# Kernel optimization log

Measured on AMD Instinct MI355X. Metric: run time of the kernel, lower is better.

The kernel has to match this reference:

```python
import jax, jax.numpy as jnp
import numpy as np

B, S, H, G, W = 4, 4096, 1024, 256, 8
CHUNK = 1024
NUM_HEADS = 4


def _ln(x, g, b, eps=1e-5):
    m = jnp.mean(x, axis=-1, keepdims=True)
    v = jnp.var(x, axis=-1, keepdims=True)
    return (x - m) / jnp.sqrt(v + eps) * g + b


def setup_inputs() -> dict:
    key = jax.random.key(0)
    ks = jax.random.split(key, 16)
    Hm = H // 2
    return {
        "x": jax.random.normal(ks[0], (B, S, H), dtype=jnp.float32),
        # wavelet params
        "mother_wavelets": jax.random.normal(ks[1], (1, W, H, 1), dtype=jnp.float32) * 0.02,
        "scales": jnp.ones((1, W, 1, 1), dtype=jnp.float32),
        # coeff_mixer: Linear(W,H/2) -> LN -> GELU -> Linear(H/2,H)  (weights stored as (in,out))
        "mix_w1": jax.random.normal(ks[2], (W, Hm), dtype=jnp.float32) * 0.02,
        "mix_b1": jnp.zeros((Hm,), dtype=jnp.float32),
        "mix_ln_g": jnp.ones((Hm,), dtype=jnp.float32),
        "mix_ln_b": jnp.zeros((Hm,), dtype=jnp.float32),
        "mix_w2": jax.random.normal(ks[3], (Hm, H), dtype=jnp.float32) * 0.02,
        "mix_b2": jnp.zeros((H,), dtype=jnp.float32),
        # attention (no bias)
        "wq": jax.random.normal(ks[4], (H, H), dtype=jnp.float32) * 0.02,
        "wk": jax.random.normal(ks[5], (H, H), dtype=jnp.float32) * 0.02,
        "wv": jax.random.normal(ks[6], (H, H), dtype=jnp.float32) * 0.02,
        "wo": jax.random.normal(ks[7], (H, H), dtype=jnp.float32) * 0.02,
        # output_proj: LN -> Linear(H, G)
        "out_ln_g": jnp.ones((H,), dtype=jnp.float32),
        "out_ln_b": jnp.zeros((H,), dtype=jnp.float32),
        "out_w": jax.random.normal(ks[8], (H, G), dtype=jnp.float32) * 0.02,
        "out_b": jnp.zeros((G,), dtype=jnp.float32),
    }


def reference(x, mother_wavelets, scales, mix_w1, mix_b1, mix_ln_g, mix_ln_b,
              mix_w2, mix_b2, wq, wk, wv, wo, out_ln_g, out_ln_b, out_w, out_b):
    b, s, h = x.shape
    nc = s // CHUNK  # chunks are independent -> fold into batch
    xc = x.reshape(b * nc, CHUNK, h)

    # wavelet coeffs: conv1d with kernel length == channels reduces to a dot product
    norm = jnp.sqrt(jnp.sum(mother_wavelets ** 2, axis=2, keepdims=True))
    kern = (mother_wavelets / jnp.maximum(norm, 1e-12)) * jax.nn.sigmoid(scales)
    kern = kern[0, :, :, 0]  # (W, H)
    coeffs = jnp.einsum('bsh,wh->bsw', xc, kern)  # (b*nc, L, W)

    # coeff mixer
    hid = _ln(coeffs @ mix_w1 + mix_b1, mix_ln_g, mix_ln_b)
    mixed = jax.nn.gelu(hid, approximate=False) @ mix_w2 + mix_b2  # (b*nc, L, H)

    # multi-head attention within each chunk (eval mode -> no causal mask)
    hd = h // NUM_HEADS
    def heads(t):
        return t.reshape(-1, CHUNK, NUM_HEADS, hd).transpose(0, 2, 1, 3)
    q, k, v = heads(mixed @ wq), heads(mixed @ wk), heads(mixed @ wv)
    scores = jnp.einsum('bhqd,bhkd->bhqk', q, k) * (hd ** -0.5)
    attn = jax.nn.softmax(scores, axis=-1)
    o = jnp.einsum('bhqk,bhkd->bhqd', attn, v)
    o = o.transpose(0, 2, 1, 3).reshape(-1, CHUNK, h) @ wo

    # output projection with residual
    y = _ln(o + mixed, out_ln_g, out_ln_b) @ out_w + out_b  # (b*nc, L, G)
    return y.reshape(b, s, -1)
```

## Files before the change

### kernel.cpp

```cpp
#include <hip/hip_runtime.h>
#include <hip/hip_bf16.h>

typedef __bf16 bf16;
typedef __bf16 bf16x4 __attribute__((ext_vector_type(4)));
typedef __bf16 bf16x8 __attribute__((ext_vector_type(8)));
typedef float f32x4 __attribute__((ext_vector_type(4)));
typedef unsigned short ushort8_t __attribute__((ext_vector_type(8)));
typedef unsigned int u32x2 __attribute__((ext_vector_type(2)));

#define GLOAD_LDS16(g, l)                                                      \
    __builtin_amdgcn_global_load_lds(                                          \
        (const __attribute__((address_space(1))) void*)(g),                    \
        (__attribute__((address_space(3))) void*)(l), 16, 0, 0)

#define LDS_ADDR(p) ((unsigned)(uintptr_t)(__attribute__((address_space(3))) void*)(p))


__global__ __launch_bounds__(256) void k_wavelet(const float* __restrict__ mw,
                                                 const float* __restrict__ sc,
                                                 float* __restrict__ kern) {
    int w = blockIdx.x;
    int tid = threadIdx.x;
    float s = 0.f;
    for (int h = tid; h < 1024; h += 256) { float v = mw[w * 1024 + h]; s += v * v; }
#pragma unroll
    for (int xm = 1; xm < 64; xm <<= 1) s += __shfl_xor(s, xm);
    __shared__ float red[4];
    if ((tid & 63) == 0) red[tid >> 6] = s;
    __syncthreads();
    float tot = red[0] + red[1] + red[2] + red[3];
    float inv = 1.f / fmaxf(sqrtf(tot), 1e-12f);
    float sg = 1.f / (1.f + __expf(-sc[w]));
    float m = inv * sg;
    for (int h = tid; h < 1024; h += 256) kern[w * 1024 + h] = mw[w * 1024 + h] * m;
}

__global__ __launch_bounds__(256) void k_coeffs(const float* __restrict__ x,
                                                const float* __restrict__ kern,
                                                float* __restrict__ coeffs) {
    __shared__ float kl[8 * 1024];
    int tid = threadIdx.x;
    for (int i = tid; i < 8192; i += 256) kl[i] = kern[i];
    __syncthreads();
    int wid = tid >> 6, lane = tid & 63;
    long row = (long)blockIdx.x * 4 + wid;
    float acc[8] = {0, 0, 0, 0, 0, 0, 0, 0};
    const float* xr = x + row * 1024;
    for (int i = 0; i < 16; i++) {
        float xv = xr[lane + i * 64];
#pragma unroll
        for (int w = 0; w < 8; w++) acc[w] += xv * kl[w * 1024 + lane + i * 64];
    }
#pragma unroll
    for (int xm = 1; xm < 64; xm <<= 1) {
#pragma unroll
        for (int w = 0; w < 8; w++) acc[w] += __shfl_xor(acc[w], xm);
    }
    if (lane == 0) {
#pragma unroll
        for (int w = 0; w < 8; w++) coeffs[row * 8 + w] = acc[w];
    }
}

__global__ __launch_bounds__(256) void k_mix1(const float* __restrict__ coeffs,
                                              const float* __restrict__ w1,
                                              const float* __restrict__ b1,
                                              const float* __restrict__ lng,
                                              const float* __restrict__ lnb,
                                              bf16* __restrict__ g) {
    long row = blockIdx.x;
    int tid = threadIdx.x;
    int wid = tid >> 6, lane = tid & 63;
    __shared__ float cf[8];
    __shared__ float red1[4], red2[4];
    if (tid < 8) cf[tid] = coeffs[row * 8 + tid];
    __syncthreads();
    float h0[2];
#pragma unroll
    for (int t = 0; t < 2; t++) {
        int j = tid + t * 256;
        float a = b1[j];
#pragma unroll
        for (int w = 0; w < 8; w++) a += cf[w] * w1[w * 512 + j];
        h0[t] = a;
    }
    float s1 = h0[0] + h0[1];
    float s2 = h0[0] * h0[0] + h0[1] * h0[1];
#pragma unroll
    for (int xm = 1; xm < 64; xm <<= 1) {
        s1 += __shfl_xor(s1, xm);
        s2 += __shfl_xor(s2, xm);
    }
    if (lane == 0) { red1[wid] = s1; red2[wid] = s2; }
    __syncthreads();
    s1 = red1[0] + red1[1] + red1[2] + red1[3];
    s2 = red2[0] + red2[1] + red2[2] + red2[3];
    float mean = s1 * (1.f / 512.f);
    float var = s2 * (1.f / 512.f) - mean * mean;
    float inv = rsqrtf(var + 1e-5f);
#pragma unroll
    for (int t = 0; t < 2; t++) {
        int j = tid + t * 256;
        float xn = (h0[t] - mean) * inv * lng[j] + lnb[j];
        float ge = 0.5f * xn * (1.f + erff(xn * 0.70710678118654752f));
        g[row * 512 + j] = (bf16)ge;
    }
}

__global__ void k_wtrans(const float* __restrict__ w, bf16* __restrict__ wt, int K, int N) {
    long idx = (long)blockIdx.x * 256 + threadIdx.x;
    if (idx < (long)K * N) {
        int kk = (int)(idx / N);
        int n = (int)(idx % N);
        wt[(long)n * K + kk] = (bf16)w[idx];
    }
}

enum { EPI_BF16 = 0, EPI_BF16_BIAS = 1, EPI_F32_BIAS = 2, EPI_VT = 3, EPI_F32 = 4 };

template <int EPI>
__global__ __launch_bounds__(512, 2) void k_gemm256(const bf16* __restrict__ A,
                                                    const bf16* __restrict__ Bt,
                                                    const float* __restrict__ bias,
                                                    void* __restrict__ Cout,
                                                    int K, int lda, int ldb, int ldc,
                                                    float scale) {
    __shared__ bf16 As[2 * 256 * 64];
    __shared__ bf16 Bs[2 * 256 * 64];
    int tid = threadIdx.x;
    int wid = tid >> 6, lane = tid & 63;
    int wr = wid >> 2, wc = wid & 3;
    long m0 = (long)blockIdx.y * 256, n0 = (long)blockIdx.x * 256;
    f32x4 acc[8][4] = {};
    const int lr = lane & 15, ko = (lane >> 4) << 3;

    const int grow = wid * 8 + (lane >> 3);
    const int gcol = (lane & 7) << 3;
    const bf16* aS = A + (m0 + grow) * lda + gcol;
    const bf16* bS = Bt + (n0 + grow) * ldb + gcol;
    bf16* lA = As + wid * 512;
    bf16* lB = Bs + wid * 512;

    const int nt = K >> 6;
#pragma unroll
    for (int i = 0; i < 4; i++) {
        GLOAD_LDS16(aS + (long)(i * 64) * lda, lA + i * 4096);
        GLOAD_LDS16(bS + (long)(i * 64) * ldb, lB + i * 4096);
    }
    __syncthreads();
    int buf = 0;
    for (int t = 0; t < nt; t++) {
        if (t + 1 < nt) {
            const int k0 = (t + 1) << 6;
            const int ob = (buf ^ 1) << 14;
#pragma unroll
            for (int i = 0; i < 4; i++) {
                GLOAD_LDS16(aS + (long)(i * 64) * lda + k0, lA + ob + i * 4096);
                GLOAD_LDS16(bS + (long)(i * 64) * ldb + k0, lB + ob + i * 4096);
            }
        }
        const bf16* At = As + (buf << 14);
        const bf16* Bb = Bs + (buf << 14);
#pragma unroll
        for (int kk = 0; kk < 2; kk++) {
            bf16x8 af[8], bfr[4];
#pragma unroll
            for (int i = 0; i < 8; i++)
                af[i] = *(const bf16x8*)&At[(wr * 128 + i * 16 + lr) * 64 + kk * 32 + ko];
#pragma unroll
            for (int j = 0; j < 4; j++)
                bfr[j] = *(const bf16x8*)&Bb[(wc * 64 + j * 16 + lr) * 64 + kk * 32 + ko];
#pragma unroll
            for (int i = 0; i < 8; i++) {
#pragma unroll
                for (int j = 0; j < 4; j++)
                    acc[i][j] = __builtin_amdgcn_mfma_f32_16x16x32_bf16(af[i], bfr[j], acc[i][j], 0, 0, 0);
            }
        }
        __syncthreads();
        buf ^= 1;
    }
    const int r0 = (lane >> 4) << 2;
#pragma unroll
    for (int i = 0; i < 8; i++) {
#pragma unroll
        for (int j = 0; j < 4; j++) {
#pragma unroll
            for (int e = 0; e < 4; e++) {
                long m = m0 + wr * 128 + i * 16 + r0 + e;
                long n = n0 + wc * 64 + j * 16 + lr;
                float v = acc[i][j][e] * scale;
                if constexpr (EPI == EPI_BF16_BIAS || EPI == EPI_F32_BIAS) v += bias[n];
                if constexpr (EPI == EPI_F32_BIAS || EPI == EPI_F32) {
                    ((float*)Cout)[m * ldc + n] = v;
                } else if constexpr (EPI == EPI_VT) {
                    long c = m >> 10, s = m & 1023, h = n >> 8, d = n & 255;
                    ((bf16*)Cout)[(((c << 2) + h) << 18) + (d << 10) + s] = (bf16)v;
                } else {
                    ((bf16*)Cout)[m * ldc + n] = (bf16)v;
                }
            }
        }
    }
}

template <int EPI>
__global__ __launch_bounds__(256) void k_gemm(const bf16* __restrict__ A,
                                              const bf16* __restrict__ Bt,
                                              const float* __restrict__ bias,
                                              void* __restrict__ Cout,
                                              int M, int N, int K,
                                              int lda, int ldb, int ldc, float scale) {
    __shared__ bf16 As[128 * 32];
    __shared__ bf16 Bs[128 * 32];
    int tid = threadIdx.x;
    int wid = tid >> 6, lane = tid & 63;
    int wr = wid >> 1, wc = wid & 1;
    long m0 = (long)blockIdx.y * 128, n0 = (long)blockIdx.x * 128;
    f32x4 acc[4][4] = {};
    const int lr = lane & 15, ko = (lane >> 4) << 3;

    const int srow = wid * 32 + (lane >> 2);
    const int scol = (lane & 3) << 3;
    const bf16* a0 = A + (m0 + srow) * lda + scol;
    const bf16* a1 = A + (m0 + srow + 16) * lda + scol;
    const bf16* b0 = Bt + (n0 + srow) * ldb + scol;
    const bf16* b1 = Bt + (n0 + srow + 16) * ldb + scol;
    bf16* la0 = As + wid * 1024;
    bf16* la1 = As + wid * 1024 + 512;
    bf16* lb0 = Bs + wid * 1024;
    bf16* lb1 = Bs + wid * 1024 + 512;

    for (int k0 = 0; k0 < K; k0 += 32) {
        GLOAD_LDS16(a0 + k0, la0);
        GLOAD_LDS16(a1 + k0, la1);
        GLOAD_LDS16(b0 + k0, lb0);
        GLOAD_LDS16(b1 + k0, lb1);
        __syncthreads();
        bf16x8 af[4], bfr[4];
#pragma unroll
        for (int i = 0; i < 4; i++)
            af[i] = *(const bf16x8*)&As[(wr * 64 + i * 16 + lr) * 32 + ko];
#pragma unroll
        for (int i = 0; i < 4; i++)
            bfr[i] = *(const bf16x8*)&Bs[(wc * 64 + i * 16 + lr) * 32 + ko];
#pragma unroll
        for (int i = 0; i < 4; i++) {
#pragma unroll
            for (int j = 0; j < 4; j++)
                acc[i][j] = __builtin_amdgcn_mfma_f32_16x16x32_bf16(af[i], bfr[j], acc[i][j], 0, 0, 0);
        }
        __syncthreads();
    }
    const int r0 = (lane >> 4) << 2;
#pragma unroll
    for (int i = 0; i < 4; i++) {
#pragma unroll
        for (int j = 0; j < 4; j++) {
#pragma unroll
            for (int e = 0; e < 4; e++) {
                long m = m0 + wr * 64 + i * 16 + r0 + e;
                long n = n0 + wc * 64 + j * 16 + lr;
                float v = acc[i][j][e] * scale;
                if constexpr (EPI == EPI_BF16_BIAS || EPI == EPI_F32_BIAS) v += bias[n];
                if constexpr (EPI == EPI_F32_BIAS || EPI == EPI_F32) {
                    ((float*)Cout)[m * ldc + n] = v;
                } else if constexpr (EPI == EPI_VT) {
                    long c = m >> 10, s = m & 1023, h = n >> 8, d = n & 255;
                    ((bf16*)Cout)[(((c << 2) + h) << 18) + (d << 10) + s] = (bf16)v;
                } else {
                    ((bf16*)Cout)[m * ldc + n] = (bf16)v;
                }
            }
        }
    }
}

__global__ __launch_bounds__(512, 2) void k_attn(const bf16* __restrict__ q,
                                                 const bf16* __restrict__ k,
                                                 const bf16* __restrict__ vt,
                                                 bf16* __restrict__ ao) {
    __shared__ __align__(16) bf16 smem[2 * 16384 + 2 * 16384 + 8192];
    bf16* Ks = smem;
    bf16* Vs = smem + 32768;
    bf16* Ps = smem + 65536;
    int tid = threadIdx.x;
    int wid = tid >> 6, lane = tid & 63;
    int c = blockIdx.x, h = blockIdx.y, q0 = blockIdx.z * 128;
    const int lr = lane & 15, gq = lane >> 4, ko = gq << 3;
    const int l7 = lr & 7;

    const int krw = wid * 2 + (lane >> 5);
    const int kg = (lane & 31) ^ (krw & 7);
    const bf16* ksrc = k + ((long)c << 10) * 1024 + h * 256 + kg * 8;
    const int vrw = wid * 8 + ((lane >> 3) & 7);
    const int vg = (lane & 7) ^ ((lane >> 3) & 7);
    const bf16* vsrc = vt + ((long)(c * 4 + h) << 18) + vg * 8;

    long qrow = ((long)c << 10) + q0 + wid * 16 + lr;
    bf16x8 qf[8];
#pragma unroll
    for (int kk = 0; kk < 8; kk++)
        qf[kk] = *(const bf16x8*)&q[qrow * 1024 + h * 256 + kk * 32 + ko];

    f32x4 oacc[16] = {};
    float m_run[4] = {-1e30f, -1e30f, -1e30f, -1e30f};
    float l_run[4] = {0.f, 0.f, 0.f, 0.f};

    bf16* PT = Ps + (wid << 10);
    const unsigned pva = LDS_ADDR(&PT[(gq << 7) + lr]);

#pragma unroll
    for (int i = 0; i < 4; i++) {
        GLOAD_LDS16(ksrc + (long)(i * 16 + krw) * 1024, Ks + i * 4096 + wid * 512);
        GLOAD_LDS16(vsrc + (long)(i * 64 + vrw) * 1024, Vs + i * 4096 + wid * 512);
    }
    __syncthreads();
    int buf = 0;
    for (int t = 0; t < 16; t++) {
        if (t < 15) {
            const int kb = (t + 1) << 6;
            const int ob = (buf ^ 1) << 14;
#pragma unroll
            for (int i = 0; i < 4; i++) {
                GLOAD_LDS16(ksrc + (long)(kb + i * 16 + krw) * 1024, Ks + ob + i * 4096 + wid * 512);
                GLOAD_LDS16(vsrc + (long)(i * 64 + vrw) * 1024 + kb, Vs + ob + i * 4096 + wid * 512);
            }
        }
        const bf16* Kc = Ks + (buf << 14);
        const bf16* Vc = Vs + (buf << 14);
        f32x4 s[4] = {};
        __builtin_amdgcn_s_setprio(1);
#pragma unroll
        for (int kk = 0; kk < 8; kk++) {
#pragma unroll
            for (int n = 0; n < 4; n++)
                s[n] = __builtin_amdgcn_mfma_f32_16x16x32_bf16(
                    qf[kk],
                    *(const bf16x8*)&Kc[((n * 16 + lr) << 8) + ((((kk << 2) + gq) ^ l7) << 3)],
                    s[n], 0, 0, 0);
        }
        __builtin_amdgcn_s_setprio(0);
        float mx[4];
#pragma unroll
        for (int e = 0; e < 4; e++)
            mx[e] = fmaxf(fmaxf(s[0][e], s[1][e]), fmaxf(s[2][e], s[3][e]));
#pragma unroll
        for (int xm = 1; xm < 16; xm <<= 1) {
#pragma unroll
            for (int e = 0; e < 4; e++) mx[e] = fmaxf(mx[e], __shfl_xor(mx[e], xm));
        }
        bool need = (mx[0] > m_run[0] + 8.f) || (mx[1] > m_run[1] + 8.f) ||
                    (mx[2] > m_run[2] + 8.f) || (mx[3] > m_run[3] + 8.f);
        if (__any(need)) {
#pragma unroll
            for (int e = 0; e < 4; e++) {
                float mn = fmaxf(m_run[e], mx[e]);
                float al = __expf(m_run[e] - mn);
                m_run[e] = mn;
                l_run[e] *= al;
#pragma unroll
                for (int f = 0; f < 16; f++) oacc[f][e] *= al;
            }
        }
        float rs[4] = {0.f, 0.f, 0.f, 0.f};
#pragma unroll
        for (int n = 0; n < 4; n++) {
#pragma unroll
            for (int e = 0; e < 4; e++) {
                float p = __expf(s[n][e] - m_run[e]);
                s[n][e] = p;
                rs[e] += p;
            }
        }
#pragma unroll
        for (int xm = 1; xm < 16; xm <<= 1) {
#pragma unroll
            for (int e = 0; e < 4; e++) rs[e] += __shfl_xor(rs[e], xm);
        }
#pragma unroll
        for (int e = 0; e < 4; e++) l_run[e] += rs[e];
#pragma unroll
        for (int n = 0; n < 4; n++) {
            bf16x4 pv = {(bf16)s[n][0], (bf16)s[n][1], (bf16)s[n][2], (bf16)s[n][3]};
            *(bf16x4*)&PT[((n * 16 + lr) << 4) + (gq << 2)] = pv;
        }
        asm volatile("s_waitcnt lgkmcnt(0)" ::: "memory");
        u32x2 t0, t1, t2, t3;
        asm volatile("ds_read_b64_tr_b16 %0, %1" : "=v"(t0) : "v"(pva));
        asm volatile("ds_read_b64_tr_b16 %0, %1 offset:128" : "=v"(t1) : "v"(pva));
        asm volatile("ds_read_b64_tr_b16 %0, %1 offset:1024" : "=v"(t2) : "v"(pva));
        asm volatile("ds_read_b64_tr_b16 %0, %1 offset:1152" : "=v"(t3) : "v"(pva));
        asm volatile("s_waitcnt lgkmcnt(0)" ::: "memory");
        __builtin_amdgcn_sched_barrier(0);
        union { u32x2 u[2]; bf16x8 v; } p0, p1;
        p0.u[0] = t0; p0.u[1] = t1;
        p1.u[0] = t2; p1.u[1] = t3;
        const bf16x8 pf0 = p0.v, pf1 = p1.v;
        __builtin_amdgcn_s_setprio(1);
#pragma unroll
        for (int n2 = 0; n2 < 16; n2++) {
            const int vrow = (n2 * 16 + lr) << 6;
            const int vswz = gq ^ l7;
            oacc[n2] = __builtin_amdgcn_mfma_f32_16x16x32_bf16(
                pf0, *(const bf16x8*)&Vc[vrow + (vswz << 3)], oacc[n2], 0, 0, 0);
            oacc[n2] = __builtin_amdgcn_mfma_f32_16x16x32_bf16(
                pf1, *(const bf16x8*)&Vc[vrow + ((vswz ^ 4) << 3)], oacc[n2], 0, 0, 0);
        }
        __builtin_amdgcn_s_setprio(0);
        __syncthreads();
        buf ^= 1;
    }
#pragma unroll
    for (int n2 = 0; n2 < 16; n2++) {
#pragma unroll
        for (int e = 0; e < 4; e++) {
            long row = ((long)c << 10) + q0 + wid * 16 + (gq << 2) + e;
            long col = ((long)h << 8) + n2 * 16 + lr;
            ao[row * 1024 + col] = (bf16)(oacc[n2][e] / l_run[e]);
        }
    }
}

__global__ __launch_bounds__(256) void k_outln(const float* __restrict__ o,
                                               const bf16* __restrict__ mixed,
                                               const float* __restrict__ g,
                                               const float* __restrict__ b,
                                               bf16* __restrict__ t) {
    long row = blockIdx.x;
    int tid = threadIdx.x;
    int wid = tid >> 6, lane = tid & 63;
    __shared__ float red1[4], red2[4];
    float x[4];
    const float* orow = o + row * 1024;
    const bf16* mrow = mixed + row * 1024;
#pragma unroll
    for (int i = 0; i < 4; i++) {
        int j = tid * 4 + i;
        x[i] = orow[j] + (float)mrow[j];
    }
    float s1 = x[0] + x[1] + x[2] + x[3];
    float s2 = x[0] * x[0] + x[1] * x[1] + x[2] * x[2] + x[3] * x[3];
#pragma unroll
    for (int xm = 1; xm < 64; xm <<= 1) {
        s1 += __shfl_xor(s1, xm);
        s2 += __shfl_xor(s2, xm);
    }
    if (lane == 0) { red1[wid] = s1; red2[wid] = s2; }
    __syncthreads();
    s1 = red1[0] + red1[1] + red1[2] + red1[3];
    s2 = red2[0] + red2[1] + red2[2] + red2[3];
    float mean = s1 * (1.f / 1024.f);
    float var = s2 * (1.f / 1024.f) - mean * mean;
    float inv = rsqrtf(var + 1e-5f);
#pragma unroll
    for (int i = 0; i < 4; i++) {
        int j = tid * 4 + i;
        t[row * 1024 + j] = (bf16)((x[i] - mean) * inv * g[j] + b[j]);
    }
}

extern "C" void kernel_launch(void* const* d_in, const int* in_sizes, int n_in,
                              void* d_out, int out_size, void* d_ws, size_t ws_size,
                              hipStream_t stream) {
    const float* x   = (const float*)d_in[0];
    const float* mw  = (const float*)d_in[1];
    const float* sc  = (const float*)d_in[2];
    const float* w1  = (const float*)d_in[3];
    const float* b1  = (const float*)d_in[4];
    const float* lng1 = (const float*)d_in[5];
    const float* lnb1 = (const float*)d_in[6];
    const float* w2  = (const float*)d_in[7];
    const float* b2  = (const float*)d_in[8];
    const float* wq  = (const float*)d_in[9];
    const float* wk  = (const float*)d_in[10];
    const float* wv  = (const float*)d_in[11];
    const float* wo  = (const float*)d_in[12];
    const float* lng2 = (const float*)d_in[13];
    const float* lnb2 = (const float*)d_in[14];
    const float* ow  = (const float*)d_in[15];
    const float* ob  = (const float*)d_in[16];

    char* p = (char*)d_ws;
    auto take = [&](size_t bytes) {
        char* r = p;
        p += (bytes + 255) & ~(size_t)255;
        return r;
    };
    const size_t M = 16384;
    float* kern   = (float*)take(8 * 1024 * sizeof(float));
    float* coeffs = (float*)take(M * 8 * sizeof(float));
    bf16* g       = (bf16*)take(M * 512 * 2);
    bf16* mixed   = (bf16*)take(M * 1024 * 2);
    bf16* qb      = (bf16*)take(M * 1024 * 2 * 2);
    bf16* kb2     = qb + M * 1024;
    float* o32    = (float*)qb;
    bf16* vtb     = (bf16*)take(M * 1024 * 2);
    bf16* tb      = vtb;
    bf16* aob     = (bf16*)take(M * 1024 * 2);
    bf16* w2t     = (bf16*)take((size_t)1024 * 512 * 2);
    bf16* wqt     = (bf16*)take((size_t)1024 * 1024 * 2);
    bf16* wkt     = (bf16*)take((size_t)1024 * 1024 * 2);
    bf16* wvt     = (bf16*)take((size_t)1024 * 1024 * 2);
    bf16* wot     = (bf16*)take((size_t)1024 * 1024 * 2);
    bf16* owt     = (bf16*)take((size_t)256 * 1024 * 2);

    k_wavelet<<<8, 256, 0, stream>>>(mw, sc, kern);
    k_coeffs<<<4096, 256, 0, stream>>>(x, kern, coeffs);
    k_mix1<<<16384, 256, 0, stream>>>(coeffs, w1, b1, lng1, lnb1, g);

    k_wtrans<<<(512 * 1024) / 256, 256, 0, stream>>>(w2, w2t, 512, 1024);
    k_wtrans<<<(1024 * 1024) / 256, 256, 0, stream>>>(wq, wqt, 1024, 1024);
    k_wtrans<<<(1024 * 1024) / 256, 256, 0, stream>>>(wk, wkt, 1024, 1024);
    k_wtrans<<<(1024 * 1024) / 256, 256, 0, stream>>>(wv, wvt, 1024, 1024);
    k_wtrans<<<(1024 * 1024) / 256, 256, 0, stream>>>(wo, wot, 1024, 1024);
    k_wtrans<<<(1024 * 256) / 256, 256, 0, stream>>>(ow, owt, 1024, 256);

    k_gemm256<EPI_BF16_BIAS><<<dim3(4, 64), 512, 0, stream>>>(
        g, w2t, b2, mixed, 512, 512, 512, 1024, 1.f);
    k_gemm256<EPI_BF16><<<dim3(4, 64), 512, 0, stream>>>(
        mixed, wqt, nullptr, qb, 1024, 1024, 1024, 1024, 0.0625f);
    k_gemm256<EPI_BF16><<<dim3(4, 64), 512, 0, stream>>>(
        mixed, wkt, nullptr, kb2, 1024, 1024, 1024, 1024, 1.f);
    k_gemm256<EPI_VT><<<dim3(4, 64), 512, 0, stream>>>(
        mixed, wvt, nullptr, vtb, 1024, 1024, 1024, 1024, 1.f);
    k_attn<<<dim3(16, 4, 8), 512, 0, stream>>>(qb, kb2, vtb, aob);
    k_gemm256<EPI_F32><<<dim3(4, 64), 512, 0, stream>>>(
        aob, wot, nullptr, o32, 1024, 1024, 1024, 1024, 1.f);
    k_outln<<<16384, 256, 0, stream>>>(o32, mixed, lng2, lnb2, tb);
    k_gemm<EPI_F32_BIAS><<<dim3(2, 128), 256, 0, stream>>>(
        tb, owt, ob, d_out, 16384, 256, 1024, 1024, 1024, 256, 1.f);
}
```

Measured before the change: 477.4 us.

## Rewrite 256x256 GEMM with 4-stage LDS pipeline, swizzle and priority hints

Replaces the double-buffered BK=64 GEMM with a four-buffer BK=32 pipeline that keeps three tiles in flight. It uses explicit vmcnt waits and raw s_barrier instead of __syncthreads. An XOR swizzle on the LDS column groups reduces bank conflicts on the fragment reads, and s_setprio raises wave priority around the MFMA block. The aim is to hide global-load latency and LDS conflicts in the projection GEMMs, at the cost of more barriers per K and hand-tuned wait counts that must match the issued loads.

```diff
diff --git a/kernel.cpp b/kernel.cpp
--- a/kernel.cpp
+++ b/kernel.cpp
@@ -119,67 +119,85 @@
 enum { EPI_BF16 = 0, EPI_BF16_BIAS = 1, EPI_F32_BIAS = 2, EPI_VT = 3, EPI_F32 = 4 };
 
 template <int EPI>
-__global__ __launch_bounds__(512, 2) void k_gemm256(const bf16* __restrict__ A,
-                                                    const bf16* __restrict__ Bt,
-                                                    const float* __restrict__ bias,
-                                                    void* __restrict__ Cout,
-                                                    int K, int lda, int ldb, int ldc,
-                                                    float scale) {
-    __shared__ bf16 As[2 * 256 * 64];
-    __shared__ bf16 Bs[2 * 256 * 64];
-    int tid = threadIdx.x;
-    int wid = tid >> 6, lane = tid & 63;
-    int wr = wid >> 2, wc = wid & 3;
-    long m0 = (long)blockIdx.y * 256, n0 = (long)blockIdx.x * 256;
+__global__ __launch_bounds__(512, 2) void k_gemm256p(const bf16* __restrict__ A,
+                                                     const bf16* __restrict__ Bt,
+                                                     const float* __restrict__ bias,
+                                                     void* __restrict__ Cout,
+                                                     int K, int lda, int ldb, int ldc,
+                                                     float scale) {
+    __shared__ bf16 As[4 * 8192];
+    __shared__ bf16 Bs[4 * 8192];
+    const int tid = threadIdx.x;
+    const int wid = tid >> 6, lane = tid & 63;
+    const int wr = wid >> 2, wc = wid & 3;
+    const long m0 = (long)blockIdx.y * 256, n0 = (long)blockIdx.x * 256;
     f32x4 acc[8][4] = {};
-    const int lr = lane & 15, ko = (lane >> 4) << 3;
-
-    const int grow = wid * 8 + (lane >> 3);
-    const int gcol = (lane & 7) << 3;
-    const bf16* aS = A + (m0 + grow) * lda + gcol;
-    const bf16* bS = Bt + (n0 + grow) * ldb + gcol;
+    const int lr = lane & 15, gq = lane >> 4;
+    const int rg = (gq ^ ((lr >> 1) & 3)) << 3;
+
+    const int srow = wid * 16 + (lane >> 2);
+    const int sg = (lane & 3) ^ ((lane >> 3) & 3);
+    const bf16* aS = A + (m0 + srow) * lda + sg * 8;
+    const bf16* bS = Bt + (n0 + srow) * ldb + sg * 8;
     bf16* lA = As + wid * 512;
     bf16* lB = Bs + wid * 512;
-
-    const int nt = K >> 6;
-#pragma unroll
-    for (int i = 0; i < 4; i++) {
-        GLOAD_LDS16(aS + (long)(i * 64) * lda, lA + i * 4096);
-        GLOAD_LDS16(bS + (long)(i * 64) * ldb, lB + i * 4096);
-    }
-    __syncthreads();
-    int buf = 0;
-    for (int t = 0; t < nt; t++) {
-        if (t + 1 < nt) {
-            const int k0 = (t + 1) << 6;
-            const int ob = (buf ^ 1) << 14;
-#pragma unroll
-            for (int i = 0; i < 4; i++) {
-                GLOAD_LDS16(aS + (long)(i * 64) * lda + k0, lA + ob + i * 4096);
-                GLOAD_LDS16(bS + (long)(i * 64) * ldb + k0, lB + ob + i * 4096);
-            }
-        }
-        const bf16* At = As + (buf << 14);
-        const bf16* Bb = Bs + (buf << 14);
-#pragma unroll
-        for (int kk = 0; kk < 2; kk++) {
-            bf16x8 af[8], bfr[4];
-#pragma unroll
-            for (int i = 0; i < 8; i++)
-                af[i] = *(const bf16x8*)&At[(wr * 128 + i * 16 + lr) * 64 + kk * 32 + ko];
+    const int nt = K >> 5;
+
+    auto stage_tile = [&](int tt) {
+        const long kq = (long)tt << 5;
+        const int ob = (tt & 3) << 13;
+        GLOAD_LDS16(aS + kq, lA + ob);
+        GLOAD_LDS16(aS + kq + (long)128 * lda, lA + ob + 4096);
+        GLOAD_LDS16(bS + kq, lB + ob);
+        GLOAD_LDS16(bS + kq + (long)128 * ldb, lB + ob + 4096);
+    };
+    auto compute_tile = [&](int bb) {
+        const bf16* At = As + (bb << 13);
+        const bf16* Bb = Bs + (bb << 13);
+        bf16x8 af[8], bfr[4];
+#pragma unroll
+        for (int i = 0; i < 8; i++)
+            af[i] = *(const bf16x8*)&At[(wr * 128 + i * 16 + lr) * 32 + rg];
+#pragma unroll
+        for (int j = 0; j < 4; j++)
+            bfr[j] = *(const bf16x8*)&Bb[(wc * 64 + j * 16 + lr) * 32 + rg];
+        __builtin_amdgcn_s_setprio(1);
+#pragma unroll
+        for (int i = 0; i < 8; i++) {
 #pragma unroll
             for (int j = 0; j < 4; j++)
-                bfr[j] = *(const bf16x8*)&Bb[(wc * 64 + j * 16 + lr) * 64 + kk * 32 + ko];
-#pragma unroll
-            for (int i = 0; i < 8; i++) {
-#pragma unroll
-                for (int j = 0; j < 4; j++)
-                    acc[i][j] = __builtin_amdgcn_mfma_f32_16x16x32_bf16(af[i], bfr[j], acc[i][j], 0, 0, 0);
-            }
-        }
-        __syncthreads();
-        buf ^= 1;
-    }
+                acc[i][j] = __builtin_amdgcn_mfma_f32_16x16x32_bf16(af[i], bfr[j], acc[i][j], 0, 0, 0);
+        }
+        __builtin_amdgcn_s_setprio(0);
+    };
+
+    stage_tile(0);
+    stage_tile(1);
+    stage_tile(2);
+    asm volatile("s_waitcnt vmcnt(8)" ::: "memory");
+    __builtin_amdgcn_sched_barrier(0);
+    __builtin_amdgcn_s_barrier();
+
+    int t = 0;
+    for (; t < nt - 3; ++t) {
+        stage_tile(t + 3);
+        compute_tile(t & 3);
+        asm volatile("s_waitcnt vmcnt(8) lgkmcnt(0)" ::: "memory");
+        __builtin_amdgcn_sched_barrier(0);
+        __builtin_amdgcn_s_barrier();
+    }
+    compute_tile(t & 3);
+    asm volatile("s_waitcnt vmcnt(4) lgkmcnt(0)" ::: "memory");
+    __builtin_amdgcn_sched_barrier(0);
+    __builtin_amdgcn_s_barrier();
+    ++t;
+    compute_tile(t & 3);
+    asm volatile("s_waitcnt vmcnt(0) lgkmcnt(0)" ::: "memory");
+    __builtin_amdgcn_sched_barrier(0);
+    __builtin_amdgcn_s_barrier();
+    ++t;
+    compute_tile(t & 3);
+
     const int r0 = (lane >> 4) << 2;
 #pragma unroll
     for (int i = 0; i < 8; i++) {
@@ -516,16 +534,16 @@
     k_wtrans<<<(1024 * 1024) / 256, 256, 0, stream>>>(wo, wot, 1024, 1024);
     k_wtrans<<<(1024 * 256) / 256, 256, 0, stream>>>(ow, owt, 1024, 256);
 
-    k_gemm256<EPI_BF16_BIAS><<<dim3(4, 64), 512, 0, stream>>>(
+    k_gemm256p<EPI_BF16_BIAS><<<dim3(4, 64), 512, 0, stream>>>(
         g, w2t, b2, mixed, 512, 512, 512, 1024, 1.f);
-    k_gemm256<EPI_BF16><<<dim3(4, 64), 512, 0, stream>>>(
+    k_gemm256p<EPI_BF16><<<dim3(4, 64), 512, 0, stream>>>(
         mixed, wqt, nullptr, qb, 1024, 1024, 1024, 1024, 0.0625f);
-    k_gemm256<EPI_BF16><<<dim3(4, 64), 512, 0, stream>>>(
+    k_gemm256p<EPI_BF16><<<dim3(4, 64), 512, 0, stream>>>(
         mixed, wkt, nullptr, kb2, 1024, 1024, 1024, 1024, 1.f);
-    k_gemm256<EPI_VT><<<dim3(4, 64), 512, 0, stream>>>(
+    k_gemm256p<EPI_VT><<<dim3(4, 64), 512, 0, stream>>>(
         mixed, wvt, nullptr, vtb, 1024, 1024, 1024, 1024, 1.f);
     k_attn<<<dim3(16, 4, 8), 512, 0, stream>>>(qb, kb2, vtb, aob);
-    k_gemm256<EPI_F32><<<dim3(4, 64), 512, 0, stream>>>(
+    k_gemm256p<EPI_F32><<<dim3(4, 64), 512, 0, stream>>>(
         aob, wot, nullptr, o32, 1024, 1024, 1024, 1024, 1.f);
     k_outln<<<16384, 256, 0, stream>>>(o32, mixed, lng2, lnb2, tb);
     k_gemm<EPI_F32_BIAS><<<dim3(2, 128), 256, 0, stream>>>(
```

Result: no change. 480.0 us (+0.5%).

## Process two query tiles per attention block to reuse K/V loads

Applied to the files above, without the earlier changes.

Each attention workgroup now handles 256 query rows, as two 128-row halves, instead of 128, so K and V tiles loaded into LDS and the K/V fragments read per MFMA are reused across both halves. The grid shrinks by half (z dimension from 8 to 4), which halves global K/V traffic per query. In exchange, register pressure doubles for the output accumulators and Q fragments under a 512-thread, 2-waves-per-SIMD launch bound, which risks spills. The grid also drops to 256 blocks, which may underfill the GPU.

```diff
diff --git a/kernel.cpp b/kernel.cpp
--- a/kernel.cpp
+++ b/kernel.cpp
@@ -280,13 +280,13 @@
                                                  const bf16* __restrict__ k,
                                                  const bf16* __restrict__ vt,
                                                  bf16* __restrict__ ao) {
-    __shared__ __align__(16) bf16 smem[2 * 16384 + 2 * 16384 + 8192];
+    __shared__ __align__(16) bf16 smem[32768 + 32768 + 8192];
     bf16* Ks = smem;
     bf16* Vs = smem + 32768;
     bf16* Ps = smem + 65536;
     int tid = threadIdx.x;
     int wid = tid >> 6, lane = tid & 63;
-    int c = blockIdx.x, h = blockIdx.y, q0 = blockIdx.z * 128;
+    int c = blockIdx.x, h = blockIdx.y, q0 = blockIdx.z * 256;
     const int lr = lane & 15, gq = lane >> 4, ko = gq << 3;
     const int l7 = lr & 7;
 
@@ -298,49 +298,24 @@
     const bf16* vsrc = vt + ((long)(c * 4 + h) << 18) + vg * 8;
 
     long qrow = ((long)c << 10) + q0 + wid * 16 + lr;
-    bf16x8 qf[8];
-#pragma unroll
-    for (int kk = 0; kk < 8; kk++)
-        qf[kk] = *(const bf16x8*)&q[qrow * 1024 + h * 256 + kk * 32 + ko];
-
-    f32x4 oacc[16] = {};
-    float m_run[4] = {-1e30f, -1e30f, -1e30f, -1e30f};
-    float l_run[4] = {0.f, 0.f, 0.f, 0.f};
+    bf16x8 qf0[8], qf1[8];
+#pragma unroll
+    for (int kk = 0; kk < 8; kk++) {
+        qf0[kk] = *(const bf16x8*)&q[qrow * 1024 + h * 256 + kk * 32 + ko];
+        qf1[kk] = *(const bf16x8*)&q[(qrow + 128) * 1024 + h * 256 + kk * 32 + ko];
+    }
+
+    f32x4 o0[16] = {}, o1[16] = {};
+    float m0r[4] = {-1e30f, -1e30f, -1e30f, -1e30f};
+    float m1r[4] = {-1e30f, -1e30f, -1e30f, -1e30f};
+    float l0r[4] = {0.f, 0.f, 0.f, 0.f};
+    float l1r[4] = {0.f, 0.f, 0.f, 0.f};
 
     bf16* PT = Ps + (wid << 10);
     const unsigned pva = LDS_ADDR(&PT[(gq << 7) + lr]);
 
-#pragma unroll
-    for (int i = 0; i < 4; i++) {
-        GLOAD_LDS16(ksrc + (long)(i * 16 + krw) * 1024, Ks + i * 4096 + wid * 512);
-        GLOAD_LDS16(vsrc + (long)(i * 64 + vrw) * 1024, Vs + i * 4096 + wid * 512);
-    }
-    __syncthreads();
-    int buf = 0;
-    for (int t = 0; t < 16; t++) {
-        if (t < 15) {
-            const int kb = (t + 1) << 6;
-            const int ob = (buf ^ 1) << 14;
-#pragma unroll
-            for (int i = 0; i < 4; i++) {
-                GLOAD_LDS16(ksrc + (long)(kb + i * 16 + krw) * 1024, Ks + ob + i * 4096 + wid * 512);
-                GLOAD_LDS16(vsrc + (long)(i * 64 + vrw) * 1024 + kb, Vs + ob + i * 4096 + wid * 512);
-            }
-        }
-        const bf16* Kc = Ks + (buf << 14);
-        const bf16* Vc = Vs + (buf << 14);
-        f32x4 s[4] = {};
-        __builtin_amdgcn_s_setprio(1);
-#pragma unroll
-        for (int kk = 0; kk < 8; kk++) {
-#pragma unroll
-            for (int n = 0; n < 4; n++)
-                s[n] = __builtin_amdgcn_mfma_f32_16x16x32_bf16(
-                    qf[kk],
-                    *(const bf16x8*)&Kc[((n * 16 + lr) << 8) + ((((kk << 2) + gq) ^ l7) << 3)],
-                    s[n], 0, 0, 0);
-        }
-        __builtin_amdgcn_s_setprio(0);
+    auto softmax_p = [&](f32x4* s, float* m_run, float* l_run, f32x4* oacc,
+                         bf16x8& pf_lo, bf16x8& pf_hi) {
         float mx[4];
 #pragma unroll
         for (int e = 0; e < 4; e++)
@@ -396,16 +371,56 @@
         union { u32x2 u[2]; bf16x8 v; } p0, p1;
         p0.u[0] = t0; p0.u[1] = t1;
         p1.u[0] = t2; p1.u[1] = t3;
-        const bf16x8 pf0 = p0.v, pf1 = p1.v;
+        pf_lo = p0.v;
+        pf_hi = p1.v;
+    };
+
+#pragma unroll
+    for (int i = 0; i < 4; i++) {
+        GLOAD_LDS16(ksrc + (long)(i * 16 + krw) * 1024, Ks + i * 4096 + wid * 512);
+        GLOAD_LDS16(vsrc + (long)(i * 64 + vrw) * 1024, Vs + i * 4096 + wid * 512);
+    }
+    __syncthreads();
+    int buf = 0;
+    for (int t = 0; t < 16; t++) {
+        if (t < 15) {
+            const int kb = (t + 1) << 6;
+            const int ob = (buf ^ 1) << 14;
+#pragma unroll
+            for (int i = 0; i < 4; i++) {
+                GLOAD_LDS16(ksrc + (long)(kb + i * 16 + krw) * 1024, Ks + ob + i * 4096 + wid * 512);
+                GLOAD_LDS16(vsrc + (long)(i * 64 + vrw) * 1024 + kb, Vs + ob + i * 4096 + wid * 512);
+            }
+        }
+        const bf16* Kc = Ks + (buf << 14);
+        const bf16* Vc = Vs + (buf << 14);
+        f32x4 s0[4] = {}, s1[4] = {};
+        __builtin_amdgcn_s_setprio(1);
+#pragma unroll
+        for (int kk = 0; kk < 8; kk++) {
+#pragma unroll
+            for (int n = 0; n < 4; n++) {
+                const bf16x8 kf =
+                    *(const bf16x8*)&Kc[((n * 16 + lr) << 8) + ((((kk << 2) + gq) ^ l7) << 3)];
+                s0[n] = __builtin_amdgcn_mfma_f32_16x16x32_bf16(qf0[kk], kf, s0[n], 0, 0, 0);
+                s1[n] = __builtin_amdgcn_mfma_f32_16x16x32_bf16(qf1[kk], kf, s1[n], 0, 0, 0);
+            }
+        }
+        __builtin_amdgcn_s_setprio(0);
+        bf16x8 pf00, pf01, pf10, pf11;
+        softmax_p(s0, m0r, l0r, o0, pf00, pf01);
+        softmax_p(s1, m1r, l1r, o1, pf10, pf11);
         __builtin_amdgcn_s_setprio(1);
 #pragma unroll
         for (int n2 = 0; n2 < 16; n2++) {
             const int vrow = (n2 * 16 + lr) << 6;
             const int vswz = gq ^ l7;
-            oacc[n2] = __builtin_amdgcn_mfma_f32_16x16x32_bf16(
-                pf0, *(const bf16x8*)&Vc[vrow + (vswz << 3)], oacc[n2], 0, 0, 0);
-            oacc[n2] = __builtin_amdgcn_mfma_f32_16x16x32_bf16(
-                pf1, *(const bf16x8*)&Vc[vrow + ((vswz ^ 4) << 3)], oacc[n2], 0, 0, 0);
+            const bf16x8 vlo = *(const bf16x8*)&Vc[vrow + (vswz << 3)];
+            const bf16x8 vhi = *(const bf16x8*)&Vc[vrow + ((vswz ^ 4) << 3)];
+            o0[n2] = __builtin_amdgcn_mfma_f32_16x16x32_bf16(pf00, vlo, o0[n2], 0, 0, 0);
+            o0[n2] = __builtin_amdgcn_mfma_f32_16x16x32_bf16(pf01, vhi, o0[n2], 0, 0, 0);
+            o1[n2] = __builtin_amdgcn_mfma_f32_16x16x32_bf16(pf10, vlo, o1[n2], 0, 0, 0);
+            o1[n2] = __builtin_amdgcn_mfma_f32_16x16x32_bf16(pf11, vhi, o1[n2], 0, 0, 0);
         }
         __builtin_amdgcn_s_setprio(0);
         __syncthreads();
@@ -417,7 +432,8 @@
         for (int e = 0; e < 4; e++) {
             long row = ((long)c << 10) + q0 + wid * 16 + (gq << 2) + e;
             long col = ((long)h << 8) + n2 * 16 + lr;
-            ao[row * 1024 + col] = (bf16)(oacc[n2][e] / l_run[e]);
+            ao[row * 1024 + col] = (bf16)(o0[n2][e] / l0r[e]);
+            ao[(row + 128) * 1024 + col] = (bf16)(o1[n2][e] / l1r[e]);
         }
     }
 }
@@ -524,7 +540,7 @@
         mixed, wkt, nullptr, kb2, 1024, 1024, 1024, 1024, 1.f);
     k_gemm256<EPI_VT><<<dim3(4, 64), 512, 0, stream>>>(
         mixed, wvt, nullptr, vtb, 1024, 1024, 1024, 1024, 1.f);
-    k_attn<<<dim3(16, 4, 8), 512, 0, stream>>>(qb, kb2, vtb, aob);
+    k_attn<<<dim3(16, 4, 4), 512, 0, stream>>>(qb, kb2, vtb, aob);
     k_gemm256<EPI_F32><<<dim3(4, 64), 512, 0, stream>>>(
         aob, wot, nullptr, o32, 1024, 1024, 1024, 1024, 1.f);
     k_outln<<<16384, 256, 0, stream>>>(o32, mixed, lng2, lnb2, tb);
```

After: 571.9 us. 1.2x slower.
